# Kernel optimization log

Hardware: AMD Instinct MI355X
Metric: run time of the kernel (lower is better)

Reference implementation:

```python
import jax, jax.numpy as jnp
import numpy as np
import math

GROUPS = 32  # min(256 // 4, 32)
EPS = 1e-5

def group_norm(x, w, b):
    B, C, H, W = x.shape
    xg = x.reshape(B, GROUPS, C // GROUPS, H, W)
    mean = jnp.mean(xg, axis=(2, 3, 4), keepdims=True)
    var = jnp.var(xg, axis=(2, 3, 4), keepdims=True)
    xn = ((xg - mean) * jax.lax.rsqrt(var + EPS)).reshape(B, C, H, W)
    return xn * w[None, :, None, None] + b[None, :, None, None]

def nin(x, W, b):
    # 1x1 projection: [B,C,H,W] x [C,D] -> [B,D,H,W]
    return jnp.einsum('bchw,cd->bdhw', x, W) + b[None, :, None, None]

def setup_inputs() -> dict:
    key = jax.random.key(0)
    ks = jax.random.split(key, 5)
    C = 256
    scale = 1.0 / math.sqrt(C)
    return {
        'x': jax.random.normal(ks[0], (4, C, 64, 64), dtype=jnp.float32),
        'gn_w': jnp.ones((C,), jnp.float32),
        'gn_b': jnp.zeros((C,), jnp.float32),
        'Wq': jax.random.normal(ks[1], (C, C), jnp.float32) * scale,
        'bq': jnp.zeros((C,), jnp.float32),
        'Wk': jax.random.normal(ks[2], (C, C), jnp.float32) * scale,
        'bk': jnp.zeros((C,), jnp.float32),
        'Wv': jax.random.normal(ks[3], (C, C), jnp.float32) * scale,
        'bv': jnp.zeros((C,), jnp.float32),
        'Wp': jax.random.normal(ks[4], (C, C), jnp.float32) * scale,
        'bp': jnp.zeros((C,), jnp.float32),
    }

def reference(x, gn_w, gn_b, Wq, bq, Wk, bk, Wv, bv, Wp, bp):
    B, C, H, W = x.shape
    h = group_norm(x, gn_w, gn_b)
    q = nin(h, Wq, bq).reshape(B, C, H * W)
    k = nin(h, Wk, bk).reshape(B, C, H * W)
    v = nin(h, Wv, bv).reshape(B, C, H * W)
    # attention logits: [B, HW, HW]
    w = jnp.einsum('bcn,bcm->bnm', q, k) * (C ** -0.5)
    w = jax.nn.softmax(w, axis=-1)
    h_out = jnp.einsum('bnm,bcm->bcn', w, v).reshape(B, C, H, W)
    h_out = nin(h_out, Wp, bp)
    out = x + h_out
    return out / math.sqrt(2.0)  # skip_rescale=True
```

## Files before the change

### kernel.cpp

```cpp
#include <hip/hip_runtime.h>
#include <math.h>


#define BB 4
#define CCH 256
#define NSP 4096
#define EPSV 1e-5f
#define ATTN_SCALE 0.0625f
#define RSQRT2 0.70710678118654752440f
#define KSPLIT 2
#define TILES_PER_PART 32

typedef __attribute__((ext_vector_type(8))) short bf16x8;
typedef __attribute__((ext_vector_type(4))) float f32x4;

typedef __attribute__((address_space(1))) void gvoid;
typedef __attribute__((address_space(3))) void lvoid;
__device__ __forceinline__ void dma16(const void* g, void* l) {
  __builtin_amdgcn_global_load_lds((gvoid*)g, (lvoid*)l, 16, 0, 0);
}

__device__ __forceinline__ short f2bf(float f) {
  union { float f; unsigned u; } a; a.f = f;
  unsigned r = a.u + 0x7fffu + ((a.u >> 16) & 1u);
  return (short)(r >> 16);
}
__device__ __forceinline__ float bf2f(short s) {
  union { unsigned u; float f; } a;
  a.u = ((unsigned)(unsigned short)s) << 16;
  return a.f;
}
__device__ __forceinline__ unsigned cvt_pk_bf16(float lo, float hi) {
  unsigned r;
  asm("v_cvt_pk_bf16_f32 %0, %1, %2" : "=v"(r) : "v"(lo), "v"(hi));
  return r;
}

__global__ __launch_bounds__(256) void prep_all(
    const float* __restrict__ x,
    const float* __restrict__ Wq, const float* __restrict__ Wk,
    const float* __restrict__ Wv, const float* __restrict__ Wp,
    float* __restrict__ stats, short* __restrict__ wts) {
  __shared__ float T[64][65];
  int bid = blockIdx.x;
  int tid = threadIdx.x;
  if (bid < 256) {
    int b = bid >> 6, g = (bid >> 1) & 31, h = bid & 1;
    size_t base = ((size_t)b * CCH + (size_t)g * 8 + (size_t)h * 4) * NSP;
    const float4* xv = (const float4*)(x + base);
    float s = 0.f, ss = 0.f;
    for (int i = tid; i < 4096; i += 256) {
      float4 v = xv[i];
      s += (v.x + v.y) + (v.z + v.w);
      ss += (v.x * v.x + v.y * v.y) + (v.z * v.z + v.w * v.w);
    }
#pragma unroll
    for (int off = 32; off > 0; off >>= 1) {
      s += __shfl_down(s, off, 64);
      ss += __shfl_down(ss, off, 64);
    }
    int wv = tid >> 6;
    if ((tid & 63) == 0) { T[0][wv] = s; T[0][4 + wv] = ss; }
    __syncthreads();
    if (tid == 0) {
      float S = T[0][0] + T[0][1] + T[0][2] + T[0][3];
      float SS = T[0][4] + T[0][5] + T[0][6] + T[0][7];
      stats[((b * 32 + g) * 2 + h) * 2 + 0] = S;
      stats[((b * 32 + g) * 2 + h) * 2 + 1] = SS;
    }
  } else {
    int wid = bid - 256;
    int c0 = (wid & 3) * 64, d0 = ((wid >> 2) & 3) * 64;
    int wz = wid >> 4;
    const float* W = (wz == 0) ? Wq : (wz == 1) ? Wk : (wz == 2) ? Wv : Wp;
    short* wt = wts + (size_t)wz * CCH * CCH;
#pragma unroll
    for (int i = 0; i < 16; ++i) {
      int idx = tid + 256 * i;
      int row = idx >> 6, col = idx & 63;
      T[row][col] = W[(size_t)(c0 + row) * CCH + d0 + col];
    }
    __syncthreads();
#pragma unroll
    for (int i = 0; i < 16; ++i) {
      int idx = tid + 256 * i;
      int dr = idx >> 6, cc = idx & 63;
      wt[(size_t)(d0 + dr) * CCH + c0 + cc] = f2bf(T[cc][dr]);
    }
  }
}

__global__ __launch_bounds__(256) void qkvg_kernel(
    const float* __restrict__ x, const float* __restrict__ stats,
    const float* __restrict__ gw, const float* __restrict__ gb,
    const short* __restrict__ wqt, const short* __restrict__ wkt,
    const short* __restrict__ wvt,
    const float* __restrict__ bq, const float* __restrict__ bk,
    const float* __restrict__ bv,
    short* __restrict__ qo, short* __restrict__ ko, short* __restrict__ vo) {
  __shared__ __align__(16) unsigned char smem[26880];
  float* aco = (float*)smem;
  float* bco = aco + 256;
  float (*Ts)[33] = (float(*)[33])(smem + 2048);
  short* Hs = (short*)(smem + 10496);
  short* Fo = (short*)(smem + 2048);

  int bx = blockIdx.x;
  int b = bx & 3, n0 = (bx >> 2) * 32;
  int tid = threadIdx.x;
  {
    int g = tid >> 3;
    const float* sp = stats + (size_t)(b * 32 + g) * 4;
    float S = sp[0] + sp[2], SS = sp[1] + sp[3];
    float mean = S * (1.f / 32768.f);
    float var = SS * (1.f / 32768.f) - mean * mean;
    float rstd = rsqrtf(var + EPSV);
    float a = gw[tid] * rstd;
    aco[tid] = a;
    bco[tid] = gb[tid] - mean * a;
  }
  __syncthreads();
  const float* xb = x + (size_t)b * CCH * NSP;
  for (int p = 0; p < 4; ++p) {
    int c0 = p * 64;
#pragma unroll
    for (int i = 0; i < 2; ++i) {
      int crow = (tid >> 3) + i * 32;
      int c = c0 + crow;
      float4 v = *(const float4*)&xb[(size_t)c * NSP + n0 + (tid & 7) * 4];
      float a = aco[c], bb = bco[c];
      v.x = v.x * a + bb; v.y = v.y * a + bb;
      v.z = v.z * a + bb; v.w = v.w * a + bb;
      *(float4*)&Ts[crow][(tid & 7) * 4] = v;
    }
    __syncthreads();
    {
      int n = tid >> 3, seg = tid & 7;
      int cb = seg * 8;
      bf16x8 r;
#pragma unroll
      for (int j = 0; j < 8; ++j) r[j] = f2bf(Ts[cb + j][n]);
      int chunk = p * 8 + seg;
      *(bf16x8*)(Hs + n * 256 + ((chunk ^ (n & 7)) * 8)) = r;
    }
    __syncthreads();
  }
  int w = tid >> 6, lane = tid & 63, quad = lane >> 4, l16 = lane & 15;
  int wr = w & 1, h = w >> 1;
  bf16x8 a_h[8];
  {
    int row = wr * 16 + l16;
#pragma unroll
    for (int kc = 0; kc < 8; ++kc)
      a_h[kc] = *(bf16x8*)(Hs + row * 256 + (((kc * 4 + quad) ^ (row & 7)) * 8));
  }
  __syncthreads();
  for (int op = 0; op < 3; ++op) {
    const short* wt = (op == 0) ? wqt : (op == 1) ? wkt : wvt;
    const float* bias = (op == 0) ? bq : (op == 1) ? bk : bv;
    f32x4 acc[8];
#pragma unroll
    for (int mb = 0; mb < 8; ++mb) acc[mb] = (f32x4){0.f, 0.f, 0.f, 0.f};
#pragma unroll 4
    for (int mb = 0; mb < 8; ++mb) {
      const short* wp = wt + (size_t)((h * 8 + mb) * 16 + l16) * CCH + quad * 8;
#pragma unroll
      for (int kc = 0; kc < 8; ++kc) {
        bf16x8 af = *(const bf16x8*)(wp + kc * 32);
        acc[mb] = __builtin_amdgcn_mfma_f32_16x16x32_bf16(af, a_h[kc], acc[mb], 0, 0, 0);
      }
    }
    int n = n0 + wr * 16 + l16;
    if (op == 2) {
      short* ob = vo + (size_t)b * CCH * NSP;
      int mm = n & 63, m0_ = n & ~63;
      int mb_ = mm >> 4, qq = (mm >> 2) & 3, rr2 = mm & 3;
      int lc = (mb_ & 1) * 4 + qq;
      int jj = (mb_ >> 1) * 4 + rr2;
      int basen = m0_ + jj;
#pragma unroll
      for (int mb = 0; mb < 8; ++mb)
#pragma unroll
        for (int r = 0; r < 4; ++r) {
          int d = (h * 8 + mb) * 16 + quad * 4 + r;
          ob[(size_t)d * NSP + basen + ((lc ^ (d & 7)) << 3)] =
              f2bf(acc[mb][r] + bias[d]);
        }
    } else {
      float sc = (op == 0) ? ATTN_SCALE : 1.f;
      int nl = wr * 16 + l16;
#pragma unroll
      for (int mb = 0; mb < 8; ++mb)
#pragma unroll
        for (int r = 0; r < 4; ++r) {
          int d = (h * 8 + mb) * 16 + quad * 4 + r;
          Fo[nl * 264 + d] = f2bf((acc[mb][r] + bias[d]) * sc);
        }
      __syncthreads();
      short* ob = ((op == 0) ? qo : ko) + (size_t)b * NSP * CCH;
      {
        int row = tid >> 3, seg = tid & 7, r7 = row & 7;
        short* dst = ob + (size_t)(n0 + row) * CCH + seg * 32;
#pragma unroll
        for (int i = 0; i < 4; ++i) {
          int xch = seg * 4 + i;
          int cs = (xch & 24) | ((xch & 7) ^ r7);
          *(bf16x8*)(dst + i * 8) = *(bf16x8*)(Fo + row * 264 + cs * 8);
        }
      }
      __syncthreads();
    }
  }
}

__global__ __launch_bounds__(512, 1) void attn_kernel(
    const short* __restrict__ q, const short* __restrict__ k,
    const short* __restrict__ v, short* __restrict__ po,
    float* __restrict__ pm, float* __restrict__ pl) {
  __shared__ __align__(16) unsigned char smem[131072];
  short* Ks0 = (short*)smem;
  short* Ks1 = (short*)(smem + 32768);
  short* Vs0 = (short*)(smem + 65536);
  short* Vs1 = (short*)(smem + 98304);
  short* Fo  = (short*)smem;

  int bx = blockIdx.x;
  int b = bx & 3;
  int n0 = ((bx >> 2) & 31) << 7;
  int kh = bx >> 7;
  const short* qb = q + (size_t)b * NSP * CCH;
  const short* kb = k + (size_t)b * NSP * CCH;
  const char*  vbB = (const char*)(v + (size_t)b * CCH * NSP);
  int tid = threadIdx.x;
  int w = tid >> 6, lane = tid & 63, quad = lane >> 4, l16 = lane & 15;
  int mbase = kh * TILES_PER_PART * 64;

  bf16x8 a_q[8];
#pragma unroll
  for (int p = 0; p < 2; ++p) {
#pragma unroll
    for (int i = 0; i < 4; ++i) {
      int off = tid * 16 + i * 8192;
      dma16((const char*)(qb + (size_t)(n0 + p * 64) * CCH) + off,
            (char*)Ks0 + off);
    }
    __syncthreads();
    if ((w >> 2) == p) {
      int row = (w & 3) * 16 + l16;
#pragma unroll
      for (int kc = 0; kc < 8; ++kc)
        a_q[kc] = *(bf16x8*)(Ks0 + row * 256 + (((kc * 4 + quad) ^ (row & 7)) * 8));
    }
    __syncthreads();
  }

#pragma unroll
  for (int i = 0; i < 4; ++i) {
    int off = tid * 16 + i * 8192;
    dma16((const char*)(kb + (size_t)mbase * CCH) + off, (char*)Ks0 + off);
    int c = off >> 7, inrow = off & 127;
    dma16(vbB + (size_t)c * (NSP * 2) + (size_t)mbase * 2 + inrow,
          (char*)Vs0 + off);
  }
  __syncthreads();
#pragma unroll
  for (int i = 0; i < 4; ++i) {
    int off = tid * 16 + i * 8192;
    dma16((const char*)(kb + (size_t)(mbase + 64) * CCH) + off,
          (char*)Ks1 + off);
  }
  f32x4 s_prev[4];
#pragma unroll
  for (int mb = 0; mb < 4; ++mb) s_prev[mb] = (f32x4){0.f, 0.f, 0.f, 0.f};
  __builtin_amdgcn_s_setprio(1);
#pragma unroll
  for (int kc = 0; kc < 8; ++kc) {
#pragma unroll
    for (int mb = 0; mb < 4; ++mb) {
      int row = mb * 16 + l16;
      bf16x8 kf = *(bf16x8*)(Ks0 + row * 256 + (((kc * 4 + quad) ^ (row & 7)) * 8));
      s_prev[mb] = __builtin_amdgcn_mfma_f32_16x16x32_bf16(kf, a_q[kc], s_prev[mb], 0, 0, 0);
    }
  }
  __builtin_amdgcn_s_setprio(0);

  f32x4 accO[16];
#pragma unroll
  for (int cb = 0; cb < 16; ++cb) accO[cb] = (f32x4){0.f, 0.f, 0.f, 0.f};
  float m_run = -1e30f, l_run = 0.f;
  int pc0 = quad ^ (l16 & 7);
  int pc1 = (4 + quad) ^ (l16 & 7);

#pragma unroll 1
  for (int t = 0; t < TILES_PER_PART; ++t) {
    __syncthreads();
    short* Kd = (t & 1) ? Ks1 : Ks0;
    short* Kr = (t & 1) ? Ks0 : Ks1;
    short* Vd = (t & 1) ? Vs0 : Vs1;
    short* Vr = (t & 1) ? Vs1 : Vs0;
    if (t + 2 < TILES_PER_PART) {
      const char* kp = (const char*)(kb + (size_t)(mbase + (t + 2) * 64) * CCH);
#pragma unroll
      for (int i = 0; i < 4; ++i) {
        int off = tid * 16 + i * 8192;
        dma16(kp + off, (char*)Kd + off);
      }
    }
    if (t + 1 < TILES_PER_PART) {
      int m0 = mbase + (t + 1) * 64;
#pragma unroll
      for (int i = 0; i < 4; ++i) {
        int off = tid * 16 + i * 8192;
        int c = off >> 7, inrow = off & 127;
        dma16(vbB + (size_t)c * (NSP * 2) + (size_t)m0 * 2 + inrow,
              (char*)Vd + off);
      }
    }
    f32x4 sn[4];
#pragma unroll
    for (int mb = 0; mb < 4; ++mb) sn[mb] = (f32x4){0.f, 0.f, 0.f, 0.f};
    if (t + 1 < TILES_PER_PART) {
      __builtin_amdgcn_s_setprio(1);
#pragma unroll
      for (int kc = 0; kc < 8; ++kc) {
#pragma unroll
        for (int mb = 0; mb < 4; ++mb) {
          int row = mb * 16 + l16;
          bf16x8 kf = *(bf16x8*)(Kr + row * 256 + (((kc * 4 + quad) ^ (row & 7)) * 8));
          sn[mb] = __builtin_amdgcn_mfma_f32_16x16x32_bf16(kf, a_q[kc], sn[mb], 0, 0, 0);
        }
      }
      __builtin_amdgcn_s_setprio(0);
    }
    float mx = -1e30f;
#pragma unroll
    for (int mb = 0; mb < 4; ++mb)
#pragma unroll
      for (int r = 0; r < 4; ++r) mx = fmaxf(mx, s_prev[mb][r]);
    mx = fmaxf(mx, __shfl_xor(mx, 16));
    mx = fmaxf(mx, __shfl_xor(mx, 32));
    if (!__all(mx - m_run <= 8.f)) {
      float mnew = fmaxf(m_run, mx);
      float alpha = __expf(m_run - mnew);
#pragma unroll
      for (int cb = 0; cb < 16; ++cb) accO[cb] *= alpha;
      l_run *= alpha;
      m_run = mnew;
    }
    float ls = 0.f;
#pragma unroll
    for (int mb = 0; mb < 4; ++mb)
#pragma unroll
      for (int r = 0; r < 4; ++r) {
        float p = __expf(s_prev[mb][r] - m_run);
        ls += p;
        s_prev[mb][r] = p;
      }
    ls += __shfl_xor(ls, 16);
    ls += __shfl_xor(ls, 32);
    l_run += ls;
    union { unsigned u[4]; bf16x8 v; } pw0, pw1;
    pw0.u[0] = cvt_pk_bf16(s_prev[0][0], s_prev[0][1]);
    pw0.u[1] = cvt_pk_bf16(s_prev[0][2], s_prev[0][3]);
    pw0.u[2] = cvt_pk_bf16(s_prev[2][0], s_prev[2][1]);
    pw0.u[3] = cvt_pk_bf16(s_prev[2][2], s_prev[2][3]);
    pw1.u[0] = cvt_pk_bf16(s_prev[1][0], s_prev[1][1]);
    pw1.u[1] = cvt_pk_bf16(s_prev[1][2], s_prev[1][3]);
    pw1.u[2] = cvt_pk_bf16(s_prev[3][0], s_prev[3][1]);
    pw1.u[3] = cvt_pk_bf16(s_prev[3][2], s_prev[3][3]);
    __builtin_amdgcn_s_setprio(1);
#pragma unroll
    for (int cb = 0; cb < 16; ++cb) {
      bf16x8 vf = *(bf16x8*)(Vr + (cb * 16 + l16) * 64 + pc0 * 8);
      accO[cb] = __builtin_amdgcn_mfma_f32_16x16x32_bf16(vf, pw0.v, accO[cb], 0, 0, 0);
    }
#pragma unroll
    for (int cb = 0; cb < 16; ++cb) {
      bf16x8 vf = *(bf16x8*)(Vr + (cb * 16 + l16) * 64 + pc1 * 8);
      accO[cb] = __builtin_amdgcn_mfma_f32_16x16x32_bf16(vf, pw1.v, accO[cb], 0, 0, 0);
    }
    __builtin_amdgcn_s_setprio(0);
#pragma unroll
    for (int mb = 0; mb < 4; ++mb) s_prev[mb] = sn[mb];
  }
  size_t sbase = ((size_t)kh * BB + b) * NSP + n0;
  if (quad == 0) {
    pm[sbase + w * 16 + l16] = m_run;
    pl[sbase + w * 16 + l16] = l_run;
  }
  float linv = 1.f / l_run;
  short* ob = po + ((size_t)kh * BB + b) * NSP * CCH;
#pragma unroll
  for (int p = 0; p < 2; ++p) {
    __syncthreads();
    if ((w >> 2) == p) {
      int nloc = (w & 3) * 16 + l16;
#pragma unroll
      for (int cb = 0; cb < 16; ++cb)
#pragma unroll
        for (int r = 0; r < 4; ++r)
          Fo[nloc * 264 + cb * 16 + quad * 4 + r] = f2bf(accO[cb][r] * linv);
    }
    __syncthreads();
    int row = tid >> 3, seg = tid & 7;
    int n = n0 + p * 64 + row;
#pragma unroll
    for (int i = 0; i < 4; ++i) {
      int ch = seg * 4 + i;
      *(bf16x8*)(ob + ((size_t)ch * NSP + n) * 8) =
          *(bf16x8*)(Fo + row * 264 + ch * 8);
    }
  }
}

__global__ __launch_bounds__(256) void proj_kernel(
    const short* __restrict__ po, const float* __restrict__ pm,
    const float* __restrict__ pl, const short* __restrict__ wpt,
    const float* __restrict__ bp, const float* __restrict__ x,
    float* __restrict__ out) {
  int n0 = blockIdx.x * 32;
  int dh = blockIdx.y * 128;
  int b = blockIdx.z;
  int tid = threadIdx.x;
  int w = tid >> 6, lane = tid & 63, quad = lane >> 4, l16 = lane & 15;
  int ng = w & 1, hq = w >> 1;
  int n = n0 + ng * 16 + l16;
  int dbase = dh + hq * 64;

  float wgt[KSPLIT];
  {
    float m[KSPLIT];
    float M = -1e30f;
#pragma unroll
    for (int s = 0; s < KSPLIT; ++s) {
      m[s] = pm[((size_t)s * BB + b) * NSP + n];
      M = fmaxf(M, m[s]);
    }
    float wsum = 0.f;
#pragma unroll
    for (int s = 0; s < KSPLIT; ++s) {
      wgt[s] = __expf(m[s] - M) * pl[((size_t)s * BB + b) * NSP + n];
      wsum += wgt[s];
    }
    float linv = 1.f / wsum;
#pragma unroll
    for (int s = 0; s < KSPLIT; ++s) wgt[s] *= linv;
  }

  f32x4 acc[4];
#pragma unroll
  for (int mb = 0; mb < 4; ++mb) acc[mb] = (f32x4){0.f, 0.f, 0.f, 0.f};

#pragma unroll 2
  for (int kc = 0; kc < 8; ++kc) {
    int coff = kc * 32 + quad * 8;
    int ch = kc * 4 + quad;
    float e[8];
#pragma unroll
    for (int i = 0; i < 8; ++i) e[i] = 0.f;
#pragma unroll
    for (int s = 0; s < KSPLIT; ++s) {
      bf16x8 f = *(const bf16x8*)(po + ((size_t)s * BB + b) * NSP * CCH +
                                  ((size_t)ch * NSP + n) * 8);
#pragma unroll
      for (int i = 0; i < 8; ++i) e[i] += wgt[s] * bf2f(f[i]);
    }
    bf16x8 bm;
#pragma unroll
    for (int i = 0; i < 8; ++i) bm[i] = f2bf(e[i]);
#pragma unroll
    for (int mb = 0; mb < 4; ++mb) {
      bf16x8 af = *(const bf16x8*)(wpt + (size_t)(dbase + mb * 16 + l16) * CCH + coff);
      acc[mb] = __builtin_amdgcn_mfma_f32_16x16x32_bf16(af, bm, acc[mb], 0, 0, 0);
    }
  }
#pragma unroll
  for (int mb = 0; mb < 4; ++mb) {
#pragma unroll
    for (int r = 0; r < 4; ++r) {
      int d = dbase + mb * 16 + quad * 4 + r;
      size_t off = ((size_t)b * CCH + d) * NSP + n;
      out[off] = (acc[mb][r] + bp[d] + x[off]) * RSQRT2;
    }
  }
}

extern "C" void kernel_launch(void* const* d_in, const int* in_sizes, int n_in,
                              void* d_out, int out_size, void* d_ws, size_t ws_size,
                              hipStream_t stream) {
  const float* x  = (const float*)d_in[0];
  const float* gw = (const float*)d_in[1];
  const float* gb = (const float*)d_in[2];
  const float* Wq = (const float*)d_in[3];
  const float* bq = (const float*)d_in[4];
  const float* Wk = (const float*)d_in[5];
  const float* bk = (const float*)d_in[6];
  const float* Wv = (const float*)d_in[7];
  const float* bv = (const float*)d_in[8];
  const float* Wp = (const float*)d_in[9];
  const float* bp = (const float*)d_in[10];
  float* out = (float*)d_out;

  const size_t SZ = (size_t)BB * CCH * NSP;
  short* qb  = (short*)d_ws;
  short* kb  = qb + SZ;
  short* vb  = kb + SZ;
  short* poT = vb + SZ;
  float* pm  = (float*)(poT + (size_t)KSPLIT * SZ);
  float* pl  = pm + (size_t)KSPLIT * BB * NSP;
  float* stats = pl + (size_t)KSPLIT * BB * NSP;
  short* wts = (short*)(stats + BB * 128);
  short* wqt = wts;
  short* wkt = wts + (size_t)CCH * CCH;
  short* wvt = wts + (size_t)2 * CCH * CCH;
  short* wpt = wts + (size_t)3 * CCH * CCH;

  prep_all<<<dim3(320), dim3(256), 0, stream>>>(x, Wq, Wk, Wv, Wp, stats, wts);
  qkvg_kernel<<<dim3(512), dim3(256), 0, stream>>>(
      x, stats, gw, gb, wqt, wkt, wvt, bq, bk, bv, qb, kb, vb);
  attn_kernel<<<dim3(BB * 32 * KSPLIT), dim3(512), 0, stream>>>(
      qb, kb, vb, poT, pm, pl);
  proj_kernel<<<dim3(128, 2, BB), dim3(256), 0, stream>>>(
      poT, pm, pl, wpt, bp, x, out);
}
```

Measured before the change: 257.5 us.

## Give each attention wave two query tiles and split keys four ways

Each attention block now handles 256 queries instead of 128, with each wave holding two 16-row query fragments. Every K and V fragment read from LDS feeds two MFMAs, halving LDS reads per MFMA. To keep the grid size the same, the key range is split four ways instead of two, with 16 tiles per part. The one-tile-ahead QK lookahead and two-deep K prefetch are dropped for a simple double buffer. The trade-offs are higher register pressure, less overlap between QK and softmax, and twice as many partial outputs for the projection kernel to merge.

```diff
diff --git a/kernel.cpp b/kernel.cpp
--- a/kernel.cpp
+++ b/kernel.cpp
@@ -8,8 +8,8 @@
 #define EPSV 1e-5f
 #define ATTN_SCALE 0.0625f
 #define RSQRT2 0.70710678118654752440f
-#define KSPLIT 2
-#define TILES_PER_PART 32
+#define KSPLIT 4
+#define TILES_PER_PART 16
 
 typedef __attribute__((ext_vector_type(8))) short bf16x8;
 typedef __attribute__((ext_vector_type(4))) float f32x4;
@@ -226,8 +226,8 @@
 
   int bx = blockIdx.x;
   int b = bx & 3;
-  int n0 = ((bx >> 2) & 31) << 7;
-  int kh = bx >> 7;
+  int n0 = ((bx >> 2) & 15) << 8;
+  int kh = bx >> 6;
   const short* qb = q + (size_t)b * NSP * CCH;
   const short* kb = k + (size_t)b * NSP * CCH;
   const char*  vbB = (const char*)(v + (size_t)b * CCH * NSP);
@@ -235,24 +235,22 @@
   int w = tid >> 6, lane = tid & 63, quad = lane >> 4, l16 = lane & 15;
   int mbase = kh * TILES_PER_PART * 64;
 
-  bf16x8 a_q[8];
-#pragma unroll
-  for (int p = 0; p < 2; ++p) {
-#pragma unroll
-    for (int i = 0; i < 4; ++i) {
-      int off = tid * 16 + i * 8192;
-      dma16((const char*)(qb + (size_t)(n0 + p * 64) * CCH) + off,
-            (char*)Ks0 + off);
-    }
-    __syncthreads();
-    if ((w >> 2) == p) {
-      int row = (w & 3) * 16 + l16;
-#pragma unroll
-      for (int kc = 0; kc < 8; ++kc)
-        a_q[kc] = *(bf16x8*)(Ks0 + row * 256 + (((kc * 4 + quad) ^ (row & 7)) * 8));
-    }
-    __syncthreads();
-  }
+#pragma unroll
+  for (int i = 0; i < 16; ++i) {
+    int off = tid * 16 + i * 8192;
+    dma16((const char*)(qb + (size_t)n0 * CCH) + off, (char*)smem + off);
+  }
+  __syncthreads();
+  bf16x8 a_q[2][8];
+#pragma unroll
+  for (int qh = 0; qh < 2; ++qh) {
+    int row = w * 32 + qh * 16 + l16;
+#pragma unroll
+    for (int kc = 0; kc < 8; ++kc)
+      a_q[qh][kc] = *(bf16x8*)((short*)smem + row * 256 +
+                               (((kc * 4 + quad) ^ (row & 7)) * 8));
+  }
+  __syncthreads();
 
 #pragma unroll
   for (int i = 0; i < 4; ++i) {
@@ -262,144 +260,148 @@
     dma16(vbB + (size_t)c * (NSP * 2) + (size_t)mbase * 2 + inrow,
           (char*)Vs0 + off);
   }
-  __syncthreads();
-#pragma unroll
-  for (int i = 0; i < 4; ++i) {
-    int off = tid * 16 + i * 8192;
-    dma16((const char*)(kb + (size_t)(mbase + 64) * CCH) + off,
-          (char*)Ks1 + off);
-  }
-  f32x4 s_prev[4];
-#pragma unroll
-  for (int mb = 0; mb < 4; ++mb) s_prev[mb] = (f32x4){0.f, 0.f, 0.f, 0.f};
-  __builtin_amdgcn_s_setprio(1);
-#pragma unroll
-  for (int kc = 0; kc < 8; ++kc) {
-#pragma unroll
-    for (int mb = 0; mb < 4; ++mb) {
-      int row = mb * 16 + l16;
-      bf16x8 kf = *(bf16x8*)(Ks0 + row * 256 + (((kc * 4 + quad) ^ (row & 7)) * 8));
-      s_prev[mb] = __builtin_amdgcn_mfma_f32_16x16x32_bf16(kf, a_q[kc], s_prev[mb], 0, 0, 0);
-    }
-  }
-  __builtin_amdgcn_s_setprio(0);
-
-  f32x4 accO[16];
-#pragma unroll
-  for (int cb = 0; cb < 16; ++cb) accO[cb] = (f32x4){0.f, 0.f, 0.f, 0.f};
-  float m_run = -1e30f, l_run = 0.f;
+
+  f32x4 accO[16][2];
+#pragma unroll
+  for (int cb = 0; cb < 16; ++cb)
+#pragma unroll
+    for (int qh = 0; qh < 2; ++qh) accO[cb][qh] = (f32x4){0.f, 0.f, 0.f, 0.f};
+  float m_run[2] = {-1e30f, -1e30f}, l_run[2] = {0.f, 0.f};
   int pc0 = quad ^ (l16 & 7);
   int pc1 = (4 + quad) ^ (l16 & 7);
 
 #pragma unroll 1
   for (int t = 0; t < TILES_PER_PART; ++t) {
     __syncthreads();
-    short* Kd = (t & 1) ? Ks1 : Ks0;
-    short* Kr = (t & 1) ? Ks0 : Ks1;
-    short* Vd = (t & 1) ? Vs0 : Vs1;
+    short* Kr = (t & 1) ? Ks1 : Ks0;
     short* Vr = (t & 1) ? Vs1 : Vs0;
-    if (t + 2 < TILES_PER_PART) {
-      const char* kp = (const char*)(kb + (size_t)(mbase + (t + 2) * 64) * CCH);
+    if (t + 1 < TILES_PER_PART) {
+      short* Kd = (t & 1) ? Ks0 : Ks1;
+      short* Vd = (t & 1) ? Vs0 : Vs1;
+      int m0 = mbase + (t + 1) * 64;
+      const char* kp = (const char*)(kb + (size_t)m0 * CCH);
 #pragma unroll
       for (int i = 0; i < 4; ++i) {
         int off = tid * 16 + i * 8192;
         dma16(kp + off, (char*)Kd + off);
-      }
-    }
-    if (t + 1 < TILES_PER_PART) {
-      int m0 = mbase + (t + 1) * 64;
-#pragma unroll
-      for (int i = 0; i < 4; ++i) {
-        int off = tid * 16 + i * 8192;
         int c = off >> 7, inrow = off & 127;
         dma16(vbB + (size_t)c * (NSP * 2) + (size_t)m0 * 2 + inrow,
               (char*)Vd + off);
       }
     }
-    f32x4 sn[4];
-#pragma unroll
-    for (int mb = 0; mb < 4; ++mb) sn[mb] = (f32x4){0.f, 0.f, 0.f, 0.f};
-    if (t + 1 < TILES_PER_PART) {
-      __builtin_amdgcn_s_setprio(1);
-#pragma unroll
-      for (int kc = 0; kc < 8; ++kc) {
-#pragma unroll
-        for (int mb = 0; mb < 4; ++mb) {
-          int row = mb * 16 + l16;
-          bf16x8 kf = *(bf16x8*)(Kr + row * 256 + (((kc * 4 + quad) ^ (row & 7)) * 8));
-          sn[mb] = __builtin_amdgcn_mfma_f32_16x16x32_bf16(kf, a_q[kc], sn[mb], 0, 0, 0);
+    f32x4 s[4][2];
+#pragma unroll
+    for (int mb = 0; mb < 4; ++mb)
+#pragma unroll
+      for (int qh = 0; qh < 2; ++qh) s[mb][qh] = (f32x4){0.f, 0.f, 0.f, 0.f};
+    __builtin_amdgcn_s_setprio(1);
+#pragma unroll
+    for (int kc = 0; kc < 8; ++kc) {
+#pragma unroll
+      for (int mb = 0; mb < 4; ++mb) {
+        int row = mb * 16 + l16;
+        bf16x8 kf = *(bf16x8*)(Kr + row * 256 + (((kc * 4 + quad) ^ (row & 7)) * 8));
+#pragma unroll
+        for (int qh = 0; qh < 2; ++qh)
+          s[mb][qh] = __builtin_amdgcn_mfma_f32_16x16x32_bf16(
+              kf, a_q[qh][kc], s[mb][qh], 0, 0, 0);
+      }
+    }
+    __builtin_amdgcn_s_setprio(0);
+    float mx[2];
+#pragma unroll
+    for (int qh = 0; qh < 2; ++qh) {
+      float m = -1e30f;
+#pragma unroll
+      for (int mb = 0; mb < 4; ++mb)
+#pragma unroll
+        for (int r = 0; r < 4; ++r) m = fmaxf(m, s[mb][qh][r]);
+      m = fmaxf(m, __shfl_xor(m, 16));
+      m = fmaxf(m, __shfl_xor(m, 32));
+      mx[qh] = m;
+    }
+    bool grow = (mx[0] - m_run[0] > 8.f) || (mx[1] - m_run[1] > 8.f);
+    if (__any(grow)) {
+#pragma unroll
+      for (int qh = 0; qh < 2; ++qh) {
+        float mnew = fmaxf(m_run[qh], mx[qh]);
+        float alpha = __expf(m_run[qh] - mnew);
+#pragma unroll
+        for (int cb = 0; cb < 16; ++cb) accO[cb][qh] *= alpha;
+        l_run[qh] *= alpha;
+        m_run[qh] = mnew;
+      }
+    }
+#pragma unroll
+    for (int qh = 0; qh < 2; ++qh) {
+      float ls = 0.f;
+#pragma unroll
+      for (int mb = 0; mb < 4; ++mb)
+#pragma unroll
+        for (int r = 0; r < 4; ++r) {
+          float p = __expf(s[mb][qh][r] - m_run[qh]);
+          ls += p;
+          s[mb][qh][r] = p;
         }
-      }
-      __builtin_amdgcn_s_setprio(0);
-    }
-    float mx = -1e30f;
-#pragma unroll
-    for (int mb = 0; mb < 4; ++mb)
-#pragma unroll
-      for (int r = 0; r < 4; ++r) mx = fmaxf(mx, s_prev[mb][r]);
-    mx = fmaxf(mx, __shfl_xor(mx, 16));
-    mx = fmaxf(mx, __shfl_xor(mx, 32));
-    if (!__all(mx - m_run <= 8.f)) {
-      float mnew = fmaxf(m_run, mx);
-      float alpha = __expf(m_run - mnew);
-#pragma unroll
-      for (int cb = 0; cb < 16; ++cb) accO[cb] *= alpha;
-      l_run *= alpha;
-      m_run = mnew;
-    }
-    float ls = 0.f;
-#pragma unroll
-    for (int mb = 0; mb < 4; ++mb)
-#pragma unroll
-      for (int r = 0; r < 4; ++r) {
-        float p = __expf(s_prev[mb][r] - m_run);
-        ls += p;
-        s_prev[mb][r] = p;
-      }
-    ls += __shfl_xor(ls, 16);
-    ls += __shfl_xor(ls, 32);
-    l_run += ls;
-    union { unsigned u[4]; bf16x8 v; } pw0, pw1;
-    pw0.u[0] = cvt_pk_bf16(s_prev[0][0], s_prev[0][1]);
-    pw0.u[1] = cvt_pk_bf16(s_prev[0][2], s_prev[0][3]);
-    pw0.u[2] = cvt_pk_bf16(s_prev[2][0], s_prev[2][1]);
-    pw0.u[3] = cvt_pk_bf16(s_prev[2][2], s_prev[2][3]);
-    pw1.u[0] = cvt_pk_bf16(s_prev[1][0], s_prev[1][1]);
-    pw1.u[1] = cvt_pk_bf16(s_prev[1][2], s_prev[1][3]);
-    pw1.u[2] = cvt_pk_bf16(s_prev[3][0], s_prev[3][1]);
-    pw1.u[3] = cvt_pk_bf16(s_prev[3][2], s_prev[3][3]);
+      ls += __shfl_xor(ls, 16);
+      ls += __shfl_xor(ls, 32);
+      l_run[qh] += ls;
+    }
+    union { unsigned u[4]; bf16x8 v; } pw0[2], pw1[2];
+#pragma unroll
+    for (int qh = 0; qh < 2; ++qh) {
+      pw0[qh].u[0] = cvt_pk_bf16(s[0][qh][0], s[0][qh][1]);
+      pw0[qh].u[1] = cvt_pk_bf16(s[0][qh][2], s[0][qh][3]);
+      pw0[qh].u[2] = cvt_pk_bf16(s[2][qh][0], s[2][qh][1]);
+      pw0[qh].u[3] = cvt_pk_bf16(s[2][qh][2], s[2][qh][3]);
+      pw1[qh].u[0] = cvt_pk_bf16(s[1][qh][0], s[1][qh][1]);
+      pw1[qh].u[1] = cvt_pk_bf16(s[1][qh][2], s[1][qh][3]);
+      pw1[qh].u[2] = cvt_pk_bf16(s[3][qh][0], s[3][qh][1]);
+      pw1[qh].u[3] = cvt_pk_bf16(s[3][qh][2], s[3][qh][3]);
+    }
     __builtin_amdgcn_s_setprio(1);
 #pragma unroll
     for (int cb = 0; cb < 16; ++cb) {
       bf16x8 vf = *(bf16x8*)(Vr + (cb * 16 + l16) * 64 + pc0 * 8);
-      accO[cb] = __builtin_amdgcn_mfma_f32_16x16x32_bf16(vf, pw0.v, accO[cb], 0, 0, 0);
+#pragma unroll
+      for (int qh = 0; qh < 2; ++qh)
+        accO[cb][qh] = __builtin_amdgcn_mfma_f32_16x16x32_bf16(
+            vf, pw0[qh].v, accO[cb][qh], 0, 0, 0);
     }
 #pragma unroll
     for (int cb = 0; cb < 16; ++cb) {
       bf16x8 vf = *(bf16x8*)(Vr + (cb * 16 + l16) * 64 + pc1 * 8);
-      accO[cb] = __builtin_amdgcn_mfma_f32_16x16x32_bf16(vf, pw1.v, accO[cb], 0, 0, 0);
+#pragma unroll
+      for (int qh = 0; qh < 2; ++qh)
+        accO[cb][qh] = __builtin_amdgcn_mfma_f32_16x16x32_bf16(
+            vf, pw1[qh].v, accO[cb][qh], 0, 0, 0);
     }
     __builtin_amdgcn_s_setprio(0);
-#pragma unroll
-    for (int mb = 0; mb < 4; ++mb) s_prev[mb] = sn[mb];
   }
   size_t sbase = ((size_t)kh * BB + b) * NSP + n0;
   if (quad == 0) {
-    pm[sbase + w * 16 + l16] = m_run;
-    pl[sbase + w * 16 + l16] = l_run;
-  }
-  float linv = 1.f / l_run;
+#pragma unroll
+    for (int qh = 0; qh < 2; ++qh) {
+      pm[sbase + w * 32 + qh * 16 + l16] = m_run[qh];
+      pl[sbase + w * 32 + qh * 16 + l16] = l_run[qh];
+    }
+  }
   short* ob = po + ((size_t)kh * BB + b) * NSP * CCH;
 #pragma unroll
-  for (int p = 0; p < 2; ++p) {
-    __syncthreads();
-    if ((w >> 2) == p) {
-      int nloc = (w & 3) * 16 + l16;
-#pragma unroll
-      for (int cb = 0; cb < 16; ++cb)
-#pragma unroll
-        for (int r = 0; r < 4; ++r)
-          Fo[nloc * 264 + cb * 16 + quad * 4 + r] = f2bf(accO[cb][r] * linv);
+  for (int p = 0; p < 4; ++p) {
+    __syncthreads();
+    if ((w >> 1) == p) {
+#pragma unroll
+      for (int qh = 0; qh < 2; ++qh) {
+        int nloc = (w & 1) * 32 + qh * 16 + l16;
+        float linv = 1.f / l_run[qh];
+#pragma unroll
+        for (int cb = 0; cb < 16; ++cb)
+#pragma unroll
+          for (int r = 0; r < 4; ++r)
+            Fo[nloc * 264 + cb * 16 + quad * 4 + r] =
+                f2bf(accO[cb][qh][r] * linv);
+      }
     }
     __syncthreads();
     int row = tid >> 3, seg = tid & 7;
@@ -518,7 +520,7 @@
   prep_all<<<dim3(320), dim3(256), 0, stream>>>(x, Wq, Wk, Wv, Wp, stats, wts);
   qkvg_kernel<<<dim3(512), dim3(256), 0, stream>>>(
       x, stats, gw, gb, wqt, wkt, wvt, bq, bk, bv, qb, kb, vb);
-  attn_kernel<<<dim3(BB * 32 * KSPLIT), dim3(512), 0, stream>>>(
+  attn_kernel<<<dim3(BB * 16 * KSPLIT), dim3(512), 0, stream>>>(
       qb, kb, vb, poT, pm, pl);
   proj_kernel<<<dim3(128, 2, BB), dim3(256), 0, stream>>>(
       poT, pm, pl, wpt, bp, x, out);
```

Result: slower. 272.7 us (+5.9%).
